# Kernel tuning notes

Measured on AMD Instinct MI355X. Metric: run time of the kernel, lower is better.

Reference implementation:

```python
import jax, jax.numpy as jnp
import numpy as np

N_SYS = 64      # number of systems
N_ELEC = 64     # electrons per system
DIM = 256
HEADS = 8
EPS = 1e-6      # flax LayerNorm default epsilon


def _edge_indices():
    # all intra-system electron pairs (including self), block-diagonal structure
    ii, jj = np.meshgrid(np.arange(N_ELEC), np.arange(N_ELEC), indexing='ij')
    offs = (np.arange(N_SYS) * N_ELEC)[:, None, None]
    ei = (offs + ii[None]).reshape(-1).astype(np.int32)
    ej = (offs + jj[None]).reshape(-1).astype(np.int32)
    return jnp.asarray(ei), jnp.asarray(ej)


def setup_inputs() -> dict:
    key = jax.random.key(0)
    ks = jax.random.split(key, 8)
    n = N_SYS * N_ELEC
    ei, ej = _edge_indices()
    s = 1.0 / np.sqrt(DIM)
    return {
        'h_one': jax.random.normal(ks[0], (n, DIM), jnp.float32),
        'W_qkv': jax.random.normal(ks[1], (DIM, 3 * DIM), jnp.float32) * s,
        'W_out': jax.random.normal(ks[2], (DIM, DIM), jnp.float32) * s,
        'ln1_scale': jnp.ones((DIM,), jnp.float32),
        'ln1_bias': jnp.zeros((DIM,), jnp.float32),
        'W_mlp': jax.random.normal(ks[3], (DIM, DIM), jnp.float32) * s,
        'b_mlp': jnp.zeros((DIM,), jnp.float32),
        'ln2_scale': jnp.ones((DIM,), jnp.float32),
        'ln2_bias': jnp.zeros((DIM,), jnp.float32),
        'e_e_i': ei,
        'e_e_j': ej,
    }


def _layernorm(x, scale, bias):
    mu = jnp.mean(x, axis=-1, keepdims=True)
    var = jnp.mean(jnp.square(x - mu), axis=-1, keepdims=True)
    return (x - mu) * jax.lax.rsqrt(var + EPS) * scale + bias


def _segment_softmax(logits, seg, n):
    mx = jax.ops.segment_max(logits, seg, num_segments=n)
    e = jnp.exp(logits - mx[seg])
    denom = jax.ops.segment_sum(e, seg, num_segments=n)
    return e / denom[seg]


def reference(h_one, W_qkv, W_out, ln1_scale, ln1_bias, W_mlp, b_mlp,
              ln2_scale, ln2_bias, e_e_i, e_e_j):
    n = h_one.shape[0]
    hd = DIM // HEADS
    qkv = h_one @ W_qkv                                  # [n, 3*dim]
    Q, K, V = jnp.split(qkv, 3, axis=-1)
    Q = Q.reshape(n, HEADS, hd)
    K = K.reshape(n, HEADS, hd)
    V = V.reshape(n, HEADS, hd)
    # per-edge attention scores: Q[i] . K[j] over head dim -> [E, H]
    A = jnp.einsum('ehd,ehd->eh', Q[e_e_i], K[e_e_j]) / jnp.sqrt(jnp.float32(hd))
    # NOTE: softmax segmented by e_e_j, scatter-sum by e_e_i (faithful to source)
    A = _segment_softmax(A, e_e_j, n)
    attn = jax.ops.segment_sum(A[..., None] * V[e_e_j], e_e_i, num_segments=n)
    attn = attn.reshape(n, DIM)
    h = h_one + attn @ W_out
    h = _layernorm(h, ln1_scale, ln1_bias)
    h = h + jax.nn.silu(h @ W_mlp + b_mlp)
    h = _layernorm(h, ln2_scale, ln2_bias)
    return h
```

## Files before the change

kernel.cpp:

```cpp
#include <hip/hip_runtime.h>
#include <hip/hip_bf16.h>
#include <math.h>

#define N_SYS   64
#define N_ELEC  64
#define NTOT    (N_SYS * N_ELEC)
#define DIM     256
#define HEADS   8
#define HDIM    32
#define LN_EPS  1e-6f

typedef __attribute__((ext_vector_type(8))) short bf16x8;
typedef __attribute__((ext_vector_type(4))) short short4v;
typedef __attribute__((ext_vector_type(4))) float f32x4;

static __device__ __forceinline__ short f2bf(float f) {
    __hip_bfloat16 h = __float2bfloat16(f);
    return *reinterpret_cast<short*>(&h);
}

__global__ __launch_bounds__(256) void prep_k(
    const float* __restrict__ Wqkv, const float* __restrict__ Wout,
    const float* __restrict__ Wmlp, short* __restrict__ WqkvT,
    short* __restrict__ WoutT, short* __restrict__ WmlpT)
{
    __shared__ float t[64][65];
    const int b = blockIdx.x;
    const float* src; short* dst; int N, tile;
    if (b < 48)      { src = Wqkv; dst = WqkvT; N = 768; tile = b; }
    else if (b < 64) { src = Wout; dst = WoutT; N = 256; tile = b - 48; }
    else             { src = Wmlp; dst = WmlpT; N = 256; tile = b - 64; }
    const int K = 256;
    const int ntN = N / 64;
    const int tk = tile / ntN, tn = tile % ntN;
    const int tid = threadIdx.x;
#pragma unroll
    for (int it = 0; it < 4; ++it) {
        int idx = it * 256 + tid;
        int r = idx >> 4, c4 = (idx & 15) * 4;
        float4 v = *(const float4*)&src[(size_t)(tk * 64 + r) * N + tn * 64 + c4];
        t[r][c4 + 0] = v.x; t[r][c4 + 1] = v.y;
        t[r][c4 + 2] = v.z; t[r][c4 + 3] = v.w;
    }
    __syncthreads();
#pragma unroll
    for (int it = 0; it < 4; ++it) {
        int idx = it * 256 + tid;
        int r = idx >> 4, c4 = (idx & 15) * 4;
        short4v o;
        o[0] = f2bf(t[c4 + 0][r]); o[1] = f2bf(t[c4 + 1][r]);
        o[2] = f2bf(t[c4 + 2][r]); o[3] = f2bf(t[c4 + 3][r]);
        *(short4v*)&dst[(size_t)(tn * 64 + r) * K + tk * 64 + c4] = o;
    }
}

__global__ __launch_bounds__(256) void k1_qkv_attn(
    const float* __restrict__ h_one, const short* __restrict__ WqkvT,
    short* __restrict__ attn)
{
    const int s = blockIdx.x >> 3;
    const int h = blockIdx.x & 7;

    __shared__ short Ha[64][72];
    __shared__ short Bs[96][72];
    __shared__ short Qs[64][40];
    __shared__ short Ks[64][40];
    __shared__ short Vt[32][72];
    __shared__ float Sm[64][68];
    __shared__ short Pm[64][72];
    __shared__ float red[8][64];

    const int tid = threadIdx.x;
    const int lane = tid & 63;
    const int w = tid >> 6;
    const int l15 = lane & 15;
    const int l4 = lane >> 4;

    const float* Abase = h_one + (size_t)s * 64 * 256;
    const short* Bbase = WqkvT + (size_t)h * 32 * 256;

    f32x4 acc[6] = {};

    for (int k0 = 0; k0 < 256; k0 += 64) {
        __syncthreads();
#pragma unroll
        for (int it = 0; it < 2; ++it) {
            int c = it * 256 + tid;
            int r = c >> 3, c8 = (c & 7) * 8;
            const float* src = &Abase[(size_t)r * 256 + k0 + c8];
            float4 v0 = *(const float4*)src;
            float4 v1 = *(const float4*)(src + 4);
            bf16x8 o;
            o[0] = f2bf(v0.x); o[1] = f2bf(v0.y); o[2] = f2bf(v0.z); o[3] = f2bf(v0.w);
            o[4] = f2bf(v1.x); o[5] = f2bf(v1.y); o[6] = f2bf(v1.z); o[7] = f2bf(v1.w);
            *(bf16x8*)&Ha[r][c8] = o;
        }
#pragma unroll
        for (int it = 0; it < 3; ++it) {
            int c = it * 256 + tid;
            int r = c >> 3, c8 = (c & 7) * 8;
            int g = r >> 5, nl = r & 31;
            *(bf16x8*)&Bs[r][c8] =
                *(const bf16x8*)&Bbase[((size_t)g * 256 + nl) * 256 + k0 + c8];
        }
        __syncthreads();
#pragma unroll
        for (int ki = 0; ki < 2; ++ki) {
            bf16x8 af = *(const bf16x8*)&Ha[w * 16 + l15][ki * 32 + l4 * 8];
#pragma unroll
            for (int nf = 0; nf < 6; ++nf) {
                bf16x8 bf = *(const bf16x8*)&Bs[nf * 16 + l15][ki * 32 + l4 * 8];
                acc[nf] = __builtin_amdgcn_mfma_f32_16x16x32_bf16(af, bf, acc[nf], 0, 0, 0);
            }
        }
    }

#pragma unroll
    for (int nf = 0; nf < 6; ++nf) {
        int c = nf * 16 + l15;
#pragma unroll
        for (int j = 0; j < 4; ++j) {
            int row = w * 16 + l4 * 4 + j;
            short v = f2bf(acc[nf][j]);
            if (c < 32)       Qs[row][c] = v;
            else if (c < 64)  Ks[row][c - 32] = v;
            else              Vt[c - 64][row] = v;
        }
    }
    __syncthreads();

    {
        const float scale = 0.17677669529663687f;
        f32x4 sacc[4] = {};
        bf16x8 aq = *(const bf16x8*)&Qs[w * 16 + l15][l4 * 8];
#pragma unroll
        for (int nf = 0; nf < 4; ++nf) {
            bf16x8 bk = *(const bf16x8*)&Ks[nf * 16 + l15][l4 * 8];
            sacc[nf] = __builtin_amdgcn_mfma_f32_16x16x32_bf16(aq, bk, sacc[nf], 0, 0, 0);
        }
#pragma unroll
        for (int nf = 0; nf < 4; ++nf)
#pragma unroll
            for (int j = 0; j < 4; ++j)
                Sm[w * 16 + l4 * 4 + j][nf * 16 + l15] = sacc[nf][j] * scale;
    }
    __syncthreads();

    {
        const int j = lane;
        const int r0 = w * 16;
        float m = -INFINITY;
#pragma unroll
        for (int r = 0; r < 16; ++r) m = fmaxf(m, Sm[r0 + r][j]);
        red[w][j] = m;
        __syncthreads();
        const float fm = fmaxf(fmaxf(red[0][j], red[1][j]), fmaxf(red[2][j], red[3][j]));
        float e[16];
        float sum = 0.0f;
#pragma unroll
        for (int r = 0; r < 16; ++r) {
            e[r] = __expf(Sm[r0 + r][j] - fm);
            sum += e[r];
        }
        red[4 + w][j] = sum;
        __syncthreads();
        const float inv = 1.0f / (red[4][j] + red[5][j] + red[6][j] + red[7][j]);
#pragma unroll
        for (int r = 0; r < 16; ++r) Pm[r0 + r][j] = f2bf(e[r] * inv);
    }
    __syncthreads();

    {
        f32x4 pv[2] = {};
#pragma unroll
        for (int ki = 0; ki < 2; ++ki) {
            bf16x8 ap = *(const bf16x8*)&Pm[w * 16 + l15][ki * 32 + l4 * 8];
#pragma unroll
            for (int nf = 0; nf < 2; ++nf) {
                bf16x8 bv = *(const bf16x8*)&Vt[nf * 16 + l15][ki * 32 + l4 * 8];
                pv[nf] = __builtin_amdgcn_mfma_f32_16x16x32_bf16(ap, bv, pv[nf], 0, 0, 0);
            }
        }
#pragma unroll
        for (int nf = 0; nf < 2; ++nf)
#pragma unroll
            for (int j = 0; j < 4; ++j) {
                int row = w * 16 + l4 * 4 + j;
                int d = nf * 16 + l15;
                attn[(size_t)(s * 64 + row) * 256 + h * 32 + d] = f2bf(pv[nf][j]);
            }
    }
}

__global__ __launch_bounds__(512) void k2_tail(
    const short* __restrict__ attnbf, const short* __restrict__ WoutT,
    const short* __restrict__ WmlpT, const float* __restrict__ h_one,
    const float* __restrict__ b_mlp,
    const float* __restrict__ ln1_s, const float* __restrict__ ln1_b,
    const float* __restrict__ ln2_s, const float* __restrict__ ln2_b,
    float* __restrict__ out)
{
    const int r0 = blockIdx.x * 16;

    __shared__ short Abf[16][264];
    __shared__ float H1[16][260];
    __shared__ short L1[16][264];

    const int tid = threadIdx.x;
    const int lane = tid & 63;
    const int w = tid >> 6;
    const int l15 = lane & 15;
    const int l4 = lane >> 4;

    {
        int r = tid >> 5, c8 = (tid & 31) * 8;
        *(bf16x8*)&Abf[r][c8] = *(const bf16x8*)&attnbf[(size_t)(r0 + r) * 256 + c8];
    }
    __syncthreads();

    f32x4 acc[2] = {};
    for (int k0 = 0; k0 < 256; k0 += 32) {
        bf16x8 af = *(const bf16x8*)&Abf[l15][k0 + l4 * 8];
#pragma unroll
        for (int nf = 0; nf < 2; ++nf) {
            int n = w * 32 + nf * 16 + l15;
            bf16x8 bf = *(const bf16x8*)&WoutT[(size_t)n * 256 + k0 + l4 * 8];
            acc[nf] = __builtin_amdgcn_mfma_f32_16x16x32_bf16(af, bf, acc[nf], 0, 0, 0);
        }
    }
#pragma unroll
    for (int nf = 0; nf < 2; ++nf) {
        int col = w * 32 + nf * 16 + l15;
#pragma unroll
        for (int j = 0; j < 4; ++j) {
            int row = l4 * 4 + j;
            H1[row][col] = acc[nf][j] + h_one[(size_t)(r0 + row) * 256 + col];
        }
    }
    __syncthreads();

    {
        float4 sc = *(const float4*)&ln1_s[lane * 4];
        float4 bi = *(const float4*)&ln1_b[lane * 4];
#pragma unroll
        for (int rr = 0; rr < 2; ++rr) {
            int row = w * 2 + rr;
            float4 v = *(const float4*)&H1[row][lane * 4];
            float su = v.x + v.y + v.z + v.w;
#pragma unroll
            for (int off = 32; off > 0; off >>= 1) su += __shfl_xor(su, off, 64);
            float mu = su * (1.0f / 256.0f);
            float dx = v.x - mu, dy = v.y - mu, dz = v.z - mu, dw = v.w - mu;
            float s2 = dx * dx + dy * dy + dz * dz + dw * dw;
#pragma unroll
            for (int off = 32; off > 0; off >>= 1) s2 += __shfl_xor(s2, off, 64);
            float inv = rsqrtf(s2 * (1.0f / 256.0f) + LN_EPS);
            float4 o;
            o.x = dx * inv * sc.x + bi.x;
            o.y = dy * inv * sc.y + bi.y;
            o.z = dz * inv * sc.z + bi.z;
            o.w = dw * inv * sc.w + bi.w;
            *(float4*)&H1[row][lane * 4] = o;
            short4v ob;
            ob[0] = f2bf(o.x); ob[1] = f2bf(o.y); ob[2] = f2bf(o.z); ob[3] = f2bf(o.w);
            *(short4v*)&L1[row][lane * 4] = ob;
        }
    }
    __syncthreads();

    f32x4 acc2[2] = {};
    for (int k0 = 0; k0 < 256; k0 += 32) {
        bf16x8 af = *(const bf16x8*)&L1[l15][k0 + l4 * 8];
#pragma unroll
        for (int nf = 0; nf < 2; ++nf) {
            int n = w * 32 + nf * 16 + l15;
            bf16x8 bf = *(const bf16x8*)&WmlpT[(size_t)n * 256 + k0 + l4 * 8];
            acc2[nf] = __builtin_amdgcn_mfma_f32_16x16x32_bf16(af, bf, acc2[nf], 0, 0, 0);
        }
    }
#pragma unroll
    for (int nf = 0; nf < 2; ++nf) {
        int col = w * 32 + nf * 16 + l15;
        float bm = b_mlp[col];
#pragma unroll
        for (int j = 0; j < 4; ++j) {
            int row = l4 * 4 + j;
            float v = acc2[nf][j] + bm;
            float sg = 1.0f / (1.0f + __expf(-v));
            H1[row][col] = H1[row][col] + v * sg;
        }
    }
    __syncthreads();

    {
        float4 sc = *(const float4*)&ln2_s[lane * 4];
        float4 bi = *(const float4*)&ln2_b[lane * 4];
#pragma unroll
        for (int rr = 0; rr < 2; ++rr) {
            int row = w * 2 + rr;
            float4 v = *(const float4*)&H1[row][lane * 4];
            float su = v.x + v.y + v.z + v.w;
#pragma unroll
            for (int off = 32; off > 0; off >>= 1) su += __shfl_xor(su, off, 64);
            float mu = su * (1.0f / 256.0f);
            float dx = v.x - mu, dy = v.y - mu, dz = v.z - mu, dw = v.w - mu;
            float s2 = dx * dx + dy * dy + dz * dz + dw * dw;
#pragma unroll
            for (int off = 32; off > 0; off >>= 1) s2 += __shfl_xor(s2, off, 64);
            float inv = rsqrtf(s2 * (1.0f / 256.0f) + LN_EPS);
            float4 o;
            o.x = dx * inv * sc.x + bi.x;
            o.y = dy * inv * sc.y + bi.y;
            o.z = dz * inv * sc.z + bi.z;
            o.w = dw * inv * sc.w + bi.w;
            *(float4*)&out[(size_t)(r0 + row) * 256 + lane * 4] = o;
        }
    }
}

extern "C" void kernel_launch(void* const* d_in, const int* in_sizes, int n_in,
                              void* d_out, int out_size, void* d_ws, size_t ws_size,
                              hipStream_t stream)
{
    const float* h_one = (const float*)d_in[0];
    const float* W_qkv = (const float*)d_in[1];
    const float* W_out = (const float*)d_in[2];
    const float* ln1_s = (const float*)d_in[3];
    const float* ln1_b = (const float*)d_in[4];
    const float* W_mlp = (const float*)d_in[5];
    const float* b_mlp = (const float*)d_in[6];
    const float* ln2_s = (const float*)d_in[7];
    const float* ln2_b = (const float*)d_in[8];
    float* out = (float*)d_out;

    char* ws = (char*)d_ws;
    short* attn_bf = (short*)ws;
    short* WqkvT   = (short*)(ws + 2097152);
    short* WoutT   = WqkvT + 768 * 256;
    short* WmlpT   = WoutT + 256 * 256;

    prep_k<<<80, 256, 0, stream>>>(W_qkv, W_out, W_mlp, WqkvT, WoutT, WmlpT);
    k1_qkv_attn<<<N_SYS * HEADS, 256, 0, stream>>>(h_one, WqkvT, attn_bf);
    k2_tail<<<NTOT / 16, 512, 0, stream>>>(attn_bf, WoutT, WmlpT, h_one, b_mlp,
                                           ln1_s, ln1_b, ln2_s, ln2_b, out);
}
```

Measured before the change: 31.01 us.

## Fuse weight prep into attention kernel and keep softmax in registers

Removes the separate weight-transpose kernel. The attention kernel now reads fp32 W_qkv directly and converts and transposes it into shared memory. The W_out and W_mlp transposes run as 32 extra blocks in the same launch. Softmax now runs on the MFMA accumulators in registers, using shuffles plus a small cross-wave reduction, instead of going through a float score matrix in shared memory. This saves one launch and some LDS traffic, but each of the 512 attention blocks now re-reads and converts fp32 weights with scattered 2-byte LDS and global stores.

Measured after the change: 27.78 us. 1.12x faster.

```diff
diff --git a/kernel.cpp b/kernel.cpp
--- a/kernel.cpp
+++ b/kernel.cpp
@@ -7,7 +7,6 @@
 #define NTOT    (N_SYS * N_ELEC)
 #define DIM     256
 #define HEADS   8
-#define HDIM    32
 #define LN_EPS  1e-6f
 
 typedef __attribute__((ext_vector_type(8))) short bf16x8;
@@ -19,45 +18,33 @@
     return *reinterpret_cast<short*>(&h);
 }
 
-__global__ __launch_bounds__(256) void prep_k(
-    const float* __restrict__ Wqkv, const float* __restrict__ Wout,
-    const float* __restrict__ Wmlp, short* __restrict__ WqkvT,
-    short* __restrict__ WoutT, short* __restrict__ WmlpT)
+__global__ __launch_bounds__(256) void k1_qkv_attn(
+    const float* __restrict__ h_one, const float* __restrict__ W_qkv,
+    const float* __restrict__ Wout, const float* __restrict__ Wmlp,
+    short* __restrict__ attn, short* __restrict__ WoutT,
+    short* __restrict__ WmlpT)
 {
-    __shared__ float t[64][65];
-    const int b = blockIdx.x;
-    const float* src; short* dst; int N, tile;
-    if (b < 48)      { src = Wqkv; dst = WqkvT; N = 768; tile = b; }
-    else if (b < 64) { src = Wout; dst = WoutT; N = 256; tile = b - 48; }
-    else             { src = Wmlp; dst = WmlpT; N = 256; tile = b - 64; }
-    const int K = 256;
-    const int ntN = N / 64;
-    const int tk = tile / ntN, tn = tile % ntN;
     const int tid = threadIdx.x;
-#pragma unroll
-    for (int it = 0; it < 4; ++it) {
-        int idx = it * 256 + tid;
-        int r = idx >> 4, c4 = (idx & 15) * 4;
-        float4 v = *(const float4*)&src[(size_t)(tk * 64 + r) * N + tn * 64 + c4];
-        t[r][c4 + 0] = v.x; t[r][c4 + 1] = v.y;
-        t[r][c4 + 2] = v.z; t[r][c4 + 3] = v.w;
-    }
-    __syncthreads();
-#pragma unroll
-    for (int it = 0; it < 4; ++it) {
-        int idx = it * 256 + tid;
-        int r = idx >> 4, c4 = (idx & 15) * 4;
-        short4v o;
-        o[0] = f2bf(t[c4 + 0][r]); o[1] = f2bf(t[c4 + 1][r]);
-        o[2] = f2bf(t[c4 + 2][r]); o[3] = f2bf(t[c4 + 3][r]);
-        *(short4v*)&dst[(size_t)(tn * 64 + r) * K + tk * 64 + c4] = o;
-    }
-}
-
-__global__ __launch_bounds__(256) void k1_qkv_attn(
-    const float* __restrict__ h_one, const short* __restrict__ WqkvT,
-    short* __restrict__ attn)
-{
+
+    if (blockIdx.x >= 512) {
+        const int b2 = blockIdx.x - 512;
+        const float* src = (b2 < 16) ? Wout : Wmlp;
+        short* dst = (b2 < 16) ? WoutT : WmlpT;
+        const int tile = b2 & 15;
+        const int tk = (tile >> 2) * 64, tn = (tile & 3) * 64;
+#pragma unroll
+        for (int p = 0; p < 4; ++p) {
+            int idx = p * 256 + tid;
+            int kk = idx >> 4, n4 = (idx & 15) * 4;
+            float4 v = *(const float4*)&src[(size_t)(tk + kk) * 256 + tn + n4];
+            dst[(size_t)(tn + n4 + 0) * 256 + tk + kk] = f2bf(v.x);
+            dst[(size_t)(tn + n4 + 1) * 256 + tk + kk] = f2bf(v.y);
+            dst[(size_t)(tn + n4 + 2) * 256 + tk + kk] = f2bf(v.z);
+            dst[(size_t)(tn + n4 + 3) * 256 + tk + kk] = f2bf(v.w);
+        }
+        return;
+    }
+
     const int s = blockIdx.x >> 3;
     const int h = blockIdx.x & 7;
 
@@ -66,18 +53,18 @@
     __shared__ short Qs[64][40];
     __shared__ short Ks[64][40];
     __shared__ short Vt[32][72];
-    __shared__ float Sm[64][68];
     __shared__ short Pm[64][72];
-    __shared__ float red[8][64];
-
-    const int tid = threadIdx.x;
+    __shared__ float redM[64][4];
+    __shared__ float redS[64][4];
+
     const int lane = tid & 63;
     const int w = tid >> 6;
     const int l15 = lane & 15;
     const int l4 = lane >> 4;
 
     const float* Abase = h_one + (size_t)s * 64 * 256;
-    const short* Bbase = WqkvT + (size_t)h * 32 * 256;
+    const int bkk = tid >> 2;
+    const int btt = tid & 3;
 
     f32x4 acc[6] = {};
 
@@ -87,21 +74,24 @@
         for (int it = 0; it < 2; ++it) {
             int c = it * 256 + tid;
             int r = c >> 3, c8 = (c & 7) * 8;
-            const float* src = &Abase[(size_t)r * 256 + k0 + c8];
-            float4 v0 = *(const float4*)src;
-            float4 v1 = *(const float4*)(src + 4);
+            const float* srcp = &Abase[(size_t)r * 256 + k0 + c8];
+            float4 v0 = *(const float4*)srcp;
+            float4 v1 = *(const float4*)(srcp + 4);
             bf16x8 o;
             o[0] = f2bf(v0.x); o[1] = f2bf(v0.y); o[2] = f2bf(v0.z); o[3] = f2bf(v0.w);
             o[4] = f2bf(v1.x); o[5] = f2bf(v1.y); o[6] = f2bf(v1.z); o[7] = f2bf(v1.w);
             *(bf16x8*)&Ha[r][c8] = o;
         }
 #pragma unroll
-        for (int it = 0; it < 3; ++it) {
-            int c = it * 256 + tid;
-            int r = c >> 3, c8 = (c & 7) * 8;
-            int g = r >> 5, nl = r & 31;
-            *(bf16x8*)&Bs[r][c8] =
-                *(const bf16x8*)&Bbase[((size_t)g * 256 + nl) * 256 + k0 + c8];
+        for (int q = 0; q < 6; ++q) {
+            int c = btt + q * 4;
+            int g = c >> 3;
+            int c4 = (c & 7) * 4;
+            float4 v = *(const float4*)&W_qkv[(size_t)(k0 + bkk) * 768 + g * 256 + h * 32 + c4];
+            Bs[g * 32 + c4 + 0][bkk] = f2bf(v.x);
+            Bs[g * 32 + c4 + 1][bkk] = f2bf(v.y);
+            Bs[g * 32 + c4 + 2][bkk] = f2bf(v.z);
+            Bs[g * 32 + c4 + 3][bkk] = f2bf(v.w);
         }
         __syncthreads();
 #pragma unroll
@@ -109,8 +99,8 @@
             bf16x8 af = *(const bf16x8*)&Ha[w * 16 + l15][ki * 32 + l4 * 8];
 #pragma unroll
             for (int nf = 0; nf < 6; ++nf) {
-                bf16x8 bf = *(const bf16x8*)&Bs[nf * 16 + l15][ki * 32 + l4 * 8];
-                acc[nf] = __builtin_amdgcn_mfma_f32_16x16x32_bf16(af, bf, acc[nf], 0, 0, 0);
+                bf16x8 bfv = *(const bf16x8*)&Bs[nf * 16 + l15][ki * 32 + l4 * 8];
+                acc[nf] = __builtin_amdgcn_mfma_f32_16x16x32_bf16(af, bfv, acc[nf], 0, 0, 0);
             }
         }
     }
@@ -129,67 +119,76 @@
     }
     __syncthreads();
 
+    const float scale = 0.17677669529663687f;
+    f32x4 sacc[4] = {};
     {
-        const float scale = 0.17677669529663687f;
-        f32x4 sacc[4] = {};
         bf16x8 aq = *(const bf16x8*)&Qs[w * 16 + l15][l4 * 8];
 #pragma unroll
         for (int nf = 0; nf < 4; ++nf) {
             bf16x8 bk = *(const bf16x8*)&Ks[nf * 16 + l15][l4 * 8];
             sacc[nf] = __builtin_amdgcn_mfma_f32_16x16x32_bf16(aq, bk, sacc[nf], 0, 0, 0);
         }
-#pragma unroll
-        for (int nf = 0; nf < 4; ++nf)
-#pragma unroll
-            for (int j = 0; j < 4; ++j)
-                Sm[w * 16 + l4 * 4 + j][nf * 16 + l15] = sacc[nf][j] * scale;
-    }
-    __syncthreads();
-
-    {
-        const int j = lane;
-        const int r0 = w * 16;
-        float m = -INFINITY;
-#pragma unroll
-        for (int r = 0; r < 16; ++r) m = fmaxf(m, Sm[r0 + r][j]);
-        red[w][j] = m;
-        __syncthreads();
-        const float fm = fmaxf(fmaxf(red[0][j], red[1][j]), fmaxf(red[2][j], red[3][j]));
-        float e[16];
-        float sum = 0.0f;
-#pragma unroll
-        for (int r = 0; r < 16; ++r) {
-            e[r] = __expf(Sm[r0 + r][j] - fm);
-            sum += e[r];
-        }
-        red[4 + w][j] = sum;
-        __syncthreads();
-        const float inv = 1.0f / (red[4][j] + red[5][j] + red[6][j] + red[7][j]);
-#pragma unroll
-        for (int r = 0; r < 16; ++r) Pm[r0 + r][j] = f2bf(e[r] * inv);
-    }
-    __syncthreads();
-
-    {
-        f32x4 pv[2] = {};
-#pragma unroll
-        for (int ki = 0; ki < 2; ++ki) {
-            bf16x8 ap = *(const bf16x8*)&Pm[w * 16 + l15][ki * 32 + l4 * 8];
-#pragma unroll
-            for (int nf = 0; nf < 2; ++nf) {
-                bf16x8 bv = *(const bf16x8*)&Vt[nf * 16 + l15][ki * 32 + l4 * 8];
-                pv[nf] = __builtin_amdgcn_mfma_f32_16x16x32_bf16(ap, bv, pv[nf], 0, 0, 0);
-            }
-        }
-#pragma unroll
-        for (int nf = 0; nf < 2; ++nf)
-#pragma unroll
-            for (int j = 0; j < 4; ++j) {
-                int row = w * 16 + l4 * 4 + j;
-                int d = nf * 16 + l15;
-                attn[(size_t)(s * 64 + row) * 256 + h * 32 + d] = f2bf(pv[nf][j]);
-            }
-    }
+    }
+    float m[4];
+#pragma unroll
+    for (int nf = 0; nf < 4; ++nf) {
+        sacc[nf] *= scale;
+        float mm = fmaxf(fmaxf(sacc[nf][0], sacc[nf][1]), fmaxf(sacc[nf][2], sacc[nf][3]));
+        mm = fmaxf(mm, __shfl_xor(mm, 16, 64));
+        mm = fmaxf(mm, __shfl_xor(mm, 32, 64));
+        m[nf] = mm;
+    }
+    if (l4 == 0) {
+#pragma unroll
+        for (int nf = 0; nf < 4; ++nf) redM[nf * 16 + l15][w] = m[nf];
+    }
+    __syncthreads();
+#pragma unroll
+    for (int nf = 0; nf < 4; ++nf) {
+        float4 mw = *(const float4*)&redM[nf * 16 + l15][0];
+        m[nf] = fmaxf(fmaxf(mw.x, mw.y), fmaxf(mw.z, mw.w));
+    }
+    float sm[4];
+#pragma unroll
+    for (int nf = 0; nf < 4; ++nf) {
+#pragma unroll
+        for (int j = 0; j < 4; ++j) sacc[nf][j] = __expf(sacc[nf][j] - m[nf]);
+        float ss = sacc[nf][0] + sacc[nf][1] + sacc[nf][2] + sacc[nf][3];
+        ss += __shfl_xor(ss, 16, 64);
+        ss += __shfl_xor(ss, 32, 64);
+        sm[nf] = ss;
+    }
+    if (l4 == 0) {
+#pragma unroll
+        for (int nf = 0; nf < 4; ++nf) redS[nf * 16 + l15][w] = sm[nf];
+    }
+    __syncthreads();
+#pragma unroll
+    for (int nf = 0; nf < 4; ++nf) {
+        float4 sw = *(const float4*)&redS[nf * 16 + l15][0];
+        float inv = 1.0f / (sw.x + sw.y + sw.z + sw.w);
+#pragma unroll
+        for (int j = 0; j < 4; ++j)
+            Pm[w * 16 + l4 * 4 + j][nf * 16 + l15] = f2bf(sacc[nf][j] * inv);
+    }
+    __syncthreads();
+
+    f32x4 pv[2] = {};
+#pragma unroll
+    for (int ki = 0; ki < 2; ++ki) {
+        bf16x8 ap = *(const bf16x8*)&Pm[w * 16 + l15][ki * 32 + l4 * 8];
+#pragma unroll
+        for (int nf = 0; nf < 2; ++nf) {
+            bf16x8 bv = *(const bf16x8*)&Vt[nf * 16 + l15][ki * 32 + l4 * 8];
+            pv[nf] = __builtin_amdgcn_mfma_f32_16x16x32_bf16(ap, bv, pv[nf], 0, 0, 0);
+        }
+    }
+#pragma unroll
+    for (int nf = 0; nf < 2; ++nf)
+#pragma unroll
+        for (int j = 0; j < 4; ++j)
+            attn[(size_t)(s * 64 + w * 16 + l4 * 4 + j) * 256 + h * 32 + nf * 16 + l15]
+                = f2bf(pv[nf][j]);
 }
 
 __global__ __launch_bounds__(512) void k2_tail(
@@ -335,12 +334,11 @@
 
     char* ws = (char*)d_ws;
     short* attn_bf = (short*)ws;
-    short* WqkvT   = (short*)(ws + 2097152);
-    short* WoutT   = WqkvT + 768 * 256;
+    short* WoutT   = (short*)(ws + 2097152);
     short* WmlpT   = WoutT + 256 * 256;
 
-    prep_k<<<80, 256, 0, stream>>>(W_qkv, W_out, W_mlp, WqkvT, WoutT, WmlpT);
-    k1_qkv_attn<<<N_SYS * HEADS, 256, 0, stream>>>(h_one, WqkvT, attn_bf);
+    k1_qkv_attn<<<512 + 32, 256, 0, stream>>>(h_one, W_qkv, W_out, W_mlp,
+                                              attn_bf, WoutT, WmlpT);
     k2_tail<<<NTOT / 16, 512, 0, stream>>>(attn_bf, WoutT, WmlpT, h_one, b_mlp,
                                            ln1_s, ln1_b, ln2_s, ln2_b, out);
 }
```
